# Kernel optimization log

Measured on AMD Instinct MI355X. Metric: run time of the kernel, lower is better.

Reference implementation:

```python
import jax, jax.numpy as jnp
import numpy as np


def setup_inputs() -> dict:
    key = jax.random.key(0)
    ks = jax.random.split(key, 5)
    B, N, C = 64, 384, 768
    return {
        "x": jax.random.normal(ks[0], (B, N, C), dtype=jnp.float32),
        "x_hsi": jax.random.normal(ks[1], (B, N, C), dtype=jnp.float32),
        "qkv_w": jax.random.normal(ks[2], (3 * C, C), dtype=jnp.float32) * 0.02,
        "proj_w": jax.random.normal(ks[3], (C, C), dtype=jnp.float32) * 0.02,
        "proj_b": jax.random.normal(ks[4], (C,), dtype=jnp.float32) * 0.02,
        "t_h": 8,
        "t_w": 8,
        "s_h": 16,
        "s_w": 16,
        "num_heads": 12,
    }


def reference(x, x_hsi, qkv_w, proj_w, proj_b, t_h, t_w, s_h, s_w, num_heads):
    B, N, C = x.shape
    H = num_heads
    Dh = C // H
    scale = Dh ** -0.5
    Lt = t_h * t_w * 2  # template tokens (2 templates)

    def qkv_heads(inp):
        qkv = (inp @ qkv_w.T).reshape(B, N, 3, H, Dh)
        qkv = jnp.transpose(qkv, (2, 0, 3, 1, 4))  # [3,B,H,N,Dh]
        return qkv[0], qkv[1], qkv[2]

    q, k, v = qkv_heads(x)
    q_hsi, k_hsi, v_hsi = qkv_heads(x_hsi)

    q_mt, q_s = q[:, :, :Lt], q[:, :, Lt:]
    k_mt, v_mt = k[:, :, :Lt], v[:, :, :Lt]
    q_s_hsi = q_hsi[:, :, Lt:]

    def attn(qq, kk, vv):
        a = jax.nn.softmax(jnp.einsum('bhqd,bhkd->bhqk', qq, kk) * scale, axis=-1)
        o = jnp.einsum('bhqk,bhkd->bhqd', a, vv)
        return jnp.transpose(o, (0, 2, 1, 3)).reshape(B, -1, C)

    x_mt = attn(q_mt, k_mt, v_mt)        # template-template
    x_s = attn(q_s, k, v)                # search attends to all
    x_s_hsi = attn(q_s_hsi, k_hsi, v_hsi)  # hsi search attends to all hsi

    out = jnp.concatenate([x_mt, x_s], axis=1) @ proj_w.T + proj_b
    out_hsi = jnp.concatenate([x_mt, x_s_hsi], axis=1) @ proj_w.T + proj_b
    return out, out_hsi
```

## Files before the change

kernel.cpp:

```cpp
#include <hip/hip_runtime.h>

typedef __attribute__((ext_vector_type(8))) short short8;
typedef __attribute__((ext_vector_type(4))) short bf16x4;
typedef __attribute__((ext_vector_type(4))) float f32x4;

__device__ __forceinline__ f32x4 mfma16(short8 a, short8 b, f32x4 c) {
  return __builtin_amdgcn_mfma_f32_16x16x32_bf16(a, b, c, 0, 0, 0);
}

__device__ __forceinline__ short f2bf(float f) {
  union { float f; unsigned u; } v; v.f = f;
  unsigned r = (v.u + 0x7fffu + ((v.u >> 16) & 1u)) >> 16;
  return (short)r;
}

__device__ __forceinline__ void gload16(const short* g, short* l) {
  __builtin_amdgcn_global_load_lds(
      (const __attribute__((address_space(1))) void*)g,
      (__attribute__((address_space(3))) void*)l, 16, 0, 0);
}

__global__ __launch_bounds__(256) void cvt_k(const float* __restrict__ src,
                                             short* __restrict__ dst, long n8) {
  long i = (long)blockIdx.x * 256 + threadIdx.x;
  const long stride = (long)gridDim.x * 256;
  for (; i < n8; i += stride) {
    float4 a = *(const float4*)(src + i * 8);
    float4 b = *(const float4*)(src + i * 8 + 4);
    short8 o = {f2bf(a.x), f2bf(a.y), f2bf(a.z), f2bf(a.w),
                f2bf(b.x), f2bf(b.y), f2bf(b.z), f2bf(b.w)};
    *(short8*)(dst + i * 8) = o;
  }
}

__device__ __forceinline__ void gemm256_core(
    const short* a00, const short* a01, const short* a10, const short* a11,
    const short* b00, const short* b01, const short* b10, const short* b11,
    char* lds, int wv, int lane, f32x4 (&acc)[8][4]) {
  const int l15 = lane & 15, q4 = lane >> 4;
  const int wm = wv & 1, wn = wv >> 1;
  const char* rdA = lds + wm * 16384;
  const char* rdB = lds + 32768 + (wn >> 1) * 16384;
  const int rB0 = (wn & 1) * 64;

  auto stg = [&](int T, int h, int tt) {
    const int t = tt >= 12 ? tt - 12 : tt;
    char* d = lds + (t & 1) * 65536 + T * 32768 + h * 16384 + wv * 2048;
    const short* g0 = T ? (h ? b10 : b00) : (h ? a10 : a00);
    const short* g1 = T ? (h ? b11 : b01) : (h ? a11 : a01);
    gload16(g0 + t * 64, (short*)d);
    gload16(g1 + t * 64, (short*)(d + 1024));
  };
  auto rdfrag = [&](const char* base, int rowl, int ks) -> short8 {
    int off = ks * 8192 + rowl * 64 + q4 * 16;
    off ^= ((off >> 9) & 1) << 5;
    return *(const short8*)(base + off);
  };

  stg(0, 0, 0); stg(0, 1, 0); stg(1, 0, 0); stg(1, 1, 0);
  stg(1, 0, 1); stg(1, 1, 1);
  asm volatile("s_waitcnt vmcnt(4)" ::: "memory");
  __builtin_amdgcn_s_barrier();

  auto ktile = [&](int buf, int t) {
    const char* A = rdA + buf * 65536;
    const char* B = rdB + buf * 65536;
    short8 afl[4], bfr[4][2];
#pragma unroll
    for (int m = 0; m < 4; ++m) afl[m] = rdfrag(A, m * 16 + l15, 0);
#pragma unroll
    for (int n = 0; n < 4; ++n) bfr[n][0] = rdfrag(B, rB0 + n * 16 + l15, 0);
    stg(0, 0, t + 1);
    __builtin_amdgcn_s_barrier();
    __builtin_amdgcn_s_setprio(1);
#pragma unroll
    for (int m = 0; m < 4; ++m)
#pragma unroll
      for (int n = 0; n < 4; ++n)
        acc[m][n] = mfma16(afl[m], bfr[n][0], acc[m][n]);
    __builtin_amdgcn_s_setprio(0);
    __builtin_amdgcn_s_barrier();
#pragma unroll
    for (int m = 0; m < 4; ++m) afl[m] = rdfrag(A, m * 16 + l15, 1);
#pragma unroll
    for (int n = 0; n < 4; ++n) bfr[n][1] = rdfrag(B, rB0 + n * 16 + l15, 1);
    stg(0, 1, t + 1);
    __builtin_amdgcn_s_barrier();
    __builtin_amdgcn_s_setprio(1);
#pragma unroll
    for (int m = 0; m < 4; ++m)
#pragma unroll
      for (int n = 0; n < 4; ++n)
        acc[m][n] = mfma16(afl[m], bfr[n][1], acc[m][n]);
    __builtin_amdgcn_s_setprio(0);
    __builtin_amdgcn_s_barrier();
#pragma unroll
    for (int m = 0; m < 4; ++m) afl[m] = rdfrag(A, (m + 4) * 16 + l15, 0);
    stg(1, 0, t + 2);
    __builtin_amdgcn_s_barrier();
    __builtin_amdgcn_s_setprio(1);
#pragma unroll
    for (int m = 0; m < 4; ++m)
#pragma unroll
      for (int n = 0; n < 4; ++n)
        acc[m + 4][n] = mfma16(afl[m], bfr[n][0], acc[m + 4][n]);
    __builtin_amdgcn_s_setprio(0);
    __builtin_amdgcn_s_barrier();
#pragma unroll
    for (int m = 0; m < 4; ++m) afl[m] = rdfrag(A, (m + 4) * 16 + l15, 1);
    stg(1, 1, t + 2);
    __builtin_amdgcn_s_barrier();
    __builtin_amdgcn_s_setprio(1);
#pragma unroll
    for (int m = 0; m < 4; ++m)
#pragma unroll
      for (int n = 0; n < 4; ++n)
        acc[m + 4][n] = mfma16(afl[m], bfr[n][1], acc[m + 4][n]);
    __builtin_amdgcn_s_setprio(0);
    asm volatile("s_waitcnt vmcnt(4)" ::: "memory");
    __builtin_amdgcn_s_barrier();
  };

  for (int g = 0; g < 6; ++g) {
    ktile(0, 2 * g);
    ktile(1, 2 * g + 1);
  }
}

__device__ __forceinline__ void stage_geom(int wv, int lane, int* srow, int* coff) {
#pragma unroll
  for (int j = 0; j < 2; ++j) {
    const int s = wv * 128 + j * 64 + lane;
    srow[j] = (s >> 2) & 127;
    coff[j] = (s >> 9) * 32 + (((((s & 3) << 4) ^ (((s >> 5) & 1) << 5))) >> 1);
  }
}

__global__ __launch_bounds__(512, 2) void gemm_qkv_k(
    const short* __restrict__ A0, const short* __restrict__ A1,
    const short* __restrict__ W,
    short* __restrict__ O0, short* __restrict__ O1) {
  extern __shared__ char lds[];
  const int tid = threadIdx.x, lane = tid & 63, wv = tid >> 6;
  const int l15 = lane & 15, q4 = lane >> 4;
  const int m0 = blockIdx.x * 256, n0 = blockIdx.y * 256;
  const short* A = blockIdx.z ? A1 : A0;
  short* O = blockIdx.z ? O1 : O0;

  int srow[2], coff[2];
  stage_geom(wv, lane, srow, coff);
  const short* a00 = A + (long)(m0 + srow[0]) * 768 + coff[0];
  const short* a01 = A + (long)(m0 + srow[1]) * 768 + coff[1];
  const short* a10 = A + (long)(m0 + 128 + srow[0]) * 768 + coff[0];
  const short* a11 = A + (long)(m0 + 128 + srow[1]) * 768 + coff[1];
  const short* b00 = W + (long)(n0 + srow[0]) * 768 + coff[0];
  const short* b01 = W + (long)(n0 + srow[1]) * 768 + coff[1];
  const short* b10 = W + (long)(n0 + 128 + srow[0]) * 768 + coff[0];
  const short* b11 = W + (long)(n0 + 128 + srow[1]) * 768 + coff[1];

  f32x4 acc[8][4] = {};
  gemm256_core(a00, a01, a10, a11, b00, b01, b10, b11, lds, wv, lane, acc);

  const int wm = wv & 1, wn = wv >> 1;
#pragma unroll
  for (int m = 0; m < 8; ++m)
#pragma unroll
    for (int n = 0; n < 4; ++n) {
      const int col = n0 + wn * 64 + n * 16 + l15;
#pragma unroll
      for (int r = 0; r < 4; ++r) {
        const int row = m0 + wm * 128 + m * 16 + q4 * 4 + r;
        O[(long)row * 2304 + col] = f2bf(acc[m][n][r]);
      }
    }
}

template <int NK, int QW>
__global__ __launch_bounds__(512, 2) void attn_f(
    const short* __restrict__ qkvx, const short* __restrict__ qkvh,
    short* __restrict__ omt, short* __restrict__ os, short* __restrict__ osh) {
  constexpr int KT = NK / 64;
  constexpr int MB = QW / 16;
  __shared__ __align__(16) short kk[2][64 * 72];
  __shared__ __align__(16) short vvs[2][64 * 72];
  __shared__ __align__(16) short sp[8][QW * 72];

  const int tid = threadIdx.x, lane = tid & 63, wv = tid >> 6;
  const int l15 = lane & 15, q4 = lane >> 4;
  const int b = blockIdx.x, h = blockIdx.y, kind = blockIdx.z;

  const short* src = kind ? qkvh : qkvx;
  short* outb;
  int q0;
  if (NK == 128) {
    outb = omt + ((long)b * 128) * 768 + h * 64;
    q0 = 0;
  } else {
    outb = (kind ? osh : os) + ((long)b * 256) * 768 + h * 64;
    q0 = 128;
  }
  const short* qb = src + ((long)(b * 384 + q0 + wv * QW)) * 2304 + h * 64;
  const short* kb = src + (long)b * 384 * 2304 + 768 + h * 64;
  const short* vb = kb + 768;

  const int key0 = tid >> 3, dg0 = tid & 7;

  short8 qf[MB][2];
#pragma unroll
  for (int m = 0; m < MB; ++m)
#pragma unroll
    for (int ks = 0; ks < 2; ++ks)
      qf[m][ks] = *(const short8*)(qb + (long)(m * 16 + l15) * 2304 + ks * 32 + q4 * 8);

  float mxr[MB][4], smr[MB][4];
  f32x4 oacc[MB][4] = {};
#pragma unroll
  for (int m = 0; m < MB; ++m)
#pragma unroll
    for (int r = 0; r < 4; ++r) { mxr[m][r] = -3e30f; smr[m][r] = 0.f; }

  short8 ka = *(const short8*)(kb + (long)key0 * 2304 + dg0 * 8);
  short8 va = *(const short8*)(vb + (long)key0 * 2304 + dg0 * 8);

  const float scale = 0.125f;
  char* spw = (char*)&sp[wv][0];

  for (int kt = 0; kt < KT; ++kt) {
    const int buf = kt & 1;
    *(short8*)&kk[buf][key0 * 72 + dg0 * 8] = ka;
    char* vt = (char*)&vvs[buf][0];
#pragma unroll
    for (int e = 0; e < 8; ++e) {
      const int d0 = dg0 * 8 + e;
      *(short*)(vt + ((d0 * 144 + key0 * 2) ^ (dg0 << 4))) = va[e];
    }
    __syncthreads();
    if (kt + 1 < KT) {
      ka = *(const short8*)(kb + (long)((kt + 1) * 64 + key0) * 2304 + dg0 * 8);
      va = *(const short8*)(vb + (long)((kt + 1) * 64 + key0) * 2304 + dg0 * 8);
    }

    f32x4 sacc[MB][4] = {};
#pragma unroll
    for (int n = 0; n < 4; ++n) {
      short8 kf0 = *(const short8*)&kk[buf][(n * 16 + l15) * 72 + q4 * 8];
      short8 kf1 = *(const short8*)&kk[buf][(n * 16 + l15) * 72 + 32 + q4 * 8];
#pragma unroll
      for (int m = 0; m < MB; ++m) {
        sacc[m][n] = mfma16(qf[m][0], kf0, sacc[m][n]);
        sacc[m][n] = mfma16(qf[m][1], kf1, sacc[m][n]);
      }
    }

#pragma unroll
    for (int m = 0; m < MB; ++m) {
      float pm[4];
#pragma unroll
      for (int r = 0; r < 4; ++r)
        pm[r] = fmaxf(fmaxf(sacc[m][0][r], sacc[m][1][r]),
                      fmaxf(sacc[m][2][r], sacc[m][3][r]));
#pragma unroll
      for (int r = 0; r < 4; ++r) {
        pm[r] = fmaxf(pm[r], __shfl_xor(pm[r], 1));
        pm[r] = fmaxf(pm[r], __shfl_xor(pm[r], 2));
        pm[r] = fmaxf(pm[r], __shfl_xor(pm[r], 4));
        pm[r] = fmaxf(pm[r], __shfl_xor(pm[r], 8));
      }
#pragma unroll
      for (int r = 0; r < 4; ++r) {
        const float mnew = fmaxf(mxr[m][r], pm[r]);
        const float resc = __expf((mxr[m][r] - mnew) * scale);
        mxr[m][r] = mnew;
        smr[m][r] *= resc;
#pragma unroll
        for (int n2 = 0; n2 < 4; ++n2) oacc[m][n2][r] *= resc;
      }
#pragma unroll
      for (int n = 0; n < 4; ++n)
#pragma unroll
        for (int r = 0; r < 4; ++r) {
          const float e = __expf((sacc[m][n][r] - mxr[m][r]) * scale);
          smr[m][r] += e;
          const int row = m * 16 + q4 * 4 + r;
          const int byte = (row * 144 + (n * 16 + l15) * 2) ^ (((row >> 3) & 1) << 5);
          *(short*)(spw + byte) = f2bf(e);
        }
    }

#pragma unroll
    for (int ks = 0; ks < 2; ++ks) {
      short8 pf[MB];
#pragma unroll
      for (int m = 0; m < MB; ++m) {
        const int row = m * 16 + l15;
        const int byte = (row * 144 + ks * 64 + q4 * 16) ^ (((row >> 3) & 1) << 5);
        pf[m] = *(const short8*)(spw + byte);
      }
#pragma unroll
      for (int n2 = 0; n2 < 4; ++n2) {
        const int db = n2 * 16 + l15;
        short8 vf = *(const short8*)(vt + ((db * 144 + (ks * 32 + q4 * 8) * 2) ^
                                           (((db >> 3) & 7) << 4)));
#pragma unroll
        for (int m = 0; m < MB; ++m)
          oacc[m][n2] = mfma16(pf[m], vf, oacc[m][n2]);
      }
    }
  }

  short* ob = outb + (long)wv * QW * 768;
#pragma unroll
  for (int m = 0; m < MB; ++m)
#pragma unroll
    for (int r = 0; r < 4; ++r) {
      float s = smr[m][r];
      s += __shfl_xor(s, 1);
      s += __shfl_xor(s, 2);
      s += __shfl_xor(s, 4);
      s += __shfl_xor(s, 8);
      const float inv = 1.f / s;
#pragma unroll
      for (int n2 = 0; n2 < 4; ++n2)
        ob[(m * 16 + q4 * 4 + r) * 768 + n2 * 16 + l15] = f2bf(oacc[m][n2][r] * inv);
    }
}

__global__ __launch_bounds__(512, 2) void gemm_proj_k(
    const short* __restrict__ mt, const short* __restrict__ sA,
    const short* __restrict__ sh,
    const short* __restrict__ W, const float* __restrict__ bias,
    float* __restrict__ out, int cb0) {
  extern __shared__ char lds[];
  const int tid = threadIdx.x, lane = tid & 63, wv = tid >> 6;
  const int l15 = lane & 15, q4 = lane >> 4;
  const int m0 = blockIdx.x * 256, n0 = blockIdx.y * 256;
  const short* s = blockIdx.z ? sh : sA;

  int srow[2], coff[2];
  stage_geom(wv, lane, srow, coff);
  auto arow = [&](int r) -> const short* {
    const int ba = r / 384, na = r % 384;
    return na < 128 ? (mt + ((long)ba * 128 + na) * 768)
                    : (s + ((long)ba * 256 + (na - 128)) * 768);
  };
  const short* a00 = arow(m0 + srow[0]) + coff[0];
  const short* a01 = arow(m0 + srow[1]) + coff[1];
  const short* a10 = arow(m0 + 128 + srow[0]) + coff[0];
  const short* a11 = arow(m0 + 128 + srow[1]) + coff[1];
  const short* b00 = W + (long)(n0 + srow[0]) * 768 + coff[0];
  const short* b01 = W + (long)(n0 + srow[1]) * 768 + coff[1];
  const short* b10 = W + (long)(n0 + 128 + srow[0]) * 768 + coff[0];
  const short* b11 = W + (long)(n0 + 128 + srow[1]) * 768 + coff[1];

  f32x4 acc[8][4] = {};
  gemm256_core(a00, a01, a10, a11, b00, b01, b10, b11, lds, wv, lane, acc);

  const int wm = wv & 1, wn = wv >> 1;
#pragma unroll
  for (int n = 0; n < 4; ++n) {
    const int col = n0 + wn * 64 + n * 16 + l15;
    const float bvv = bias[col];
#pragma unroll
    for (int m = 0; m < 8; ++m)
#pragma unroll
      for (int r = 0; r < 4; ++r) {
        const int row = m0 + wm * 128 + m * 16 + q4 * 4 + r;
        out[(long)blockIdx.z * 18874368 + ((long)cb0 * 384 + row) * 768 + col] =
            acc[m][n][r] + bvv;
      }
  }
}

extern "C" void kernel_launch(void* const* d_in, const int* in_sizes, int n_in,
                              void* d_out, int out_size, void* d_ws, size_t ws_size,
                              hipStream_t stream) {
  (void)in_sizes; (void)n_in; (void)out_size;
  const float* x  = (const float*)d_in[0];
  const float* xh = (const float*)d_in[1];
  const float* qw = (const float*)d_in[2];
  const float* pw = (const float*)d_in[3];
  const float* pb = (const float*)d_in[4];
  float* out = (float*)d_out;

  const long qwSz = 2304L * 768 * 2;
  const long pwSz = 768L * 768 * 2;
  const long fixedW = qwSz + pwSz;
  const long perBatch = (2L * 384 * 768 + 2L * 384 * 2304 + 640L * 768) * 2;
  int CB = 64;
  while (CB > 2 && (long)CB * perBatch + fixedW > (long)ws_size) CB >>= 1;

  char* ws = (char*)d_ws;
  short* qwbf = (short*)ws;
  short* pwbf = (short*)(ws + qwSz);
  char* dyn = ws + fixedW;
  const long xbfSz = (long)CB * 384 * 768 * 2;
  const long qkvSz = (long)CB * 384 * 2304 * 2;
  const long mtSz  = (long)CB * 128 * 768 * 2;
  const long sSz   = (long)CB * 256 * 768 * 2;
  short* xbf  = (short*)dyn;
  short* xhbf = (short*)(dyn + xbfSz);
  short* qkvx = (short*)(dyn + 2 * xbfSz);
  short* qkvh = (short*)(dyn + 2 * xbfSz + qkvSz);
  short* amt  = (short*)(dyn + 2 * xbfSz + 2 * qkvSz);
  short* as_  = (short*)(dyn + 2 * xbfSz + 2 * qkvSz + mtSz);
  short* ash  = (short*)(dyn + 2 * xbfSz + 2 * qkvSz + mtSz + sSz);

  cvt_k<<<864, 256, 0, stream>>>(qw, qwbf, 2304L * 768 / 8);
  cvt_k<<<288, 256, 0, stream>>>(pw, pwbf, 768L * 768 / 8);

  const int nch = 64 / CB;
  for (int c = 0; c < nch; ++c) {
    const int cb0 = c * CB;
    const long n8 = (long)CB * 384 * 768 / 8;
    cvt_k<<<2048, 256, 0, stream>>>(x + (long)cb0 * 384 * 768, xbf, n8);
    cvt_k<<<2048, 256, 0, stream>>>(xh + (long)cb0 * 384 * 768, xhbf, n8);
    dim3 g1((CB * 384) / 256, 9, 2);
    gemm_qkv_k<<<g1, 512, 131072, stream>>>(xbf, xhbf, qwbf, qkvx, qkvh);
    attn_f<128, 16><<<dim3(CB, 12, 1), 512, 0, stream>>>(qkvx, qkvh, amt, as_, ash);
    attn_f<384, 32><<<dim3(CB, 12, 2), 512, 0, stream>>>(qkvx, qkvh, amt, as_, ash);
    dim3 g3((CB * 384) / 256, 3, 2);
    gemm_proj_k<<<g3, 512, 131072, stream>>>(amt, as_, ash, pwbf, pb, out, cb0);
  }
}
```

Baseline: 666.3 us.

## Fuse fp32-to-bf16 activation conversion into QKV GEMM and skip softmax rescales

The QKV GEMM now reads fp32 activations directly, loading them into registers, converting them with packed bf16 conversion instructions and writing them into LDS. This removes the two separate conversion kernels and their bf16 workspace round trip. A-tile staging moves from async global-to-LDS loads to register loads plus LDS stores, which adds VGPR pressure and LDS write traffic to the GEMM. Separately, the attention softmax now rescales the running max only when some row's new max exceeds the stored max by a threshold, which avoids many exp and multiply operations but lets exponents grow without a rescale in between.

```diff
diff --git a/kernel.cpp b/kernel.cpp
--- a/kernel.cpp
+++ b/kernel.cpp
@@ -12,6 +12,12 @@
   union { float f; unsigned u; } v; v.f = f;
   unsigned r = (v.u + 0x7fffu + ((v.u >> 16) & 1u)) >> 16;
   return (short)r;
+}
+
+__device__ __forceinline__ unsigned cvtpk(float lo, float hi) {
+  unsigned r;
+  asm volatile("v_cvt_pk_bf16_f32 %0, %1, %2" : "=v"(r) : "v"(lo), "v"(hi));
+  return r;
 }
 
 __device__ __forceinline__ void gload16(const short* g, short* l) {
@@ -33,6 +39,157 @@
   }
 }
 
+__device__ __forceinline__ void stage_geom(int wv, int lane, int* srow, int* coff) {
+#pragma unroll
+  for (int j = 0; j < 2; ++j) {
+    const int s = wv * 128 + j * 64 + lane;
+    srow[j] = (s >> 2) & 127;
+    coff[j] = (s >> 9) * 32 + (((((s & 3) << 4) ^ (((s >> 5) & 1) << 5))) >> 1);
+  }
+}
+
+__global__ __launch_bounds__(512, 2) void gemm_qkv_k(
+    const float* __restrict__ A0, const float* __restrict__ A1,
+    const short* __restrict__ W,
+    short* __restrict__ O0, short* __restrict__ O1) {
+  extern __shared__ char lds[];
+  const int tid = threadIdx.x, lane = tid & 63, wv = tid >> 6;
+  const int l15 = lane & 15, q4 = lane >> 4;
+  const int m0 = blockIdx.x * 256, n0 = blockIdx.y * 256;
+  const float* A = blockIdx.z ? A1 : A0;
+  short* O = blockIdx.z ? O1 : O0;
+  const int wm = wv & 1, wn = wv >> 1;
+  const char* rdA = lds + wm * 16384;
+  const char* rdB = lds + 32768 + (wn >> 1) * 16384;
+  const int rB0 = (wn & 1) * 64;
+
+  const int arow = (tid >> 2) & 127, ac16 = tid & 3;
+  const int abase = (arow * 64 + ac16 * 16) ^ (((arow >> 3) & 1) << 5);
+  const float* asrcL = A + (long)(m0 + arow) * 768 + ac16 * 8;
+  const float* asrcH = A + (long)(m0 + 128 + arow) * 768 + ac16 * 8;
+
+  int srow[2], coff[2];
+  stage_geom(wv, lane, srow, coff);
+  const short* b00 = W + (long)(n0 + srow[0]) * 768 + coff[0];
+  const short* b01 = W + (long)(n0 + srow[1]) * 768 + coff[1];
+  const short* b10 = W + (long)(n0 + 128 + srow[0]) * 768 + coff[0];
+  const short* b11 = W + (long)(n0 + 128 + srow[1]) * 768 + coff[1];
+
+  auto stgB = [&](int h, int tt) {
+    const int t = tt >= 12 ? tt - 12 : tt;
+    char* d = lds + (t & 1) * 65536 + 32768 + h * 16384 + wv * 2048;
+    gload16((h ? b10 : b00) + t * 64, (short*)d);
+    gload16((h ? b11 : b01) + t * 64, (short*)(d + 1024));
+  };
+  float4 areg[4][2];
+  auto loadA = [&](int tt) {
+    const int t = tt >= 12 ? tt - 12 : tt;
+    const float* pL = asrcL + t * 64;
+    const float* pH = asrcH + t * 64;
+    areg[0][0] = *(const float4*)(pL);       areg[0][1] = *(const float4*)(pL + 4);
+    areg[1][0] = *(const float4*)(pL + 32);  areg[1][1] = *(const float4*)(pL + 36);
+    areg[2][0] = *(const float4*)(pH);       areg[2][1] = *(const float4*)(pH + 4);
+    areg[3][0] = *(const float4*)(pH + 32);  areg[3][1] = *(const float4*)(pH + 36);
+  };
+  auto writeA = [&](int tt) {
+    char* dstb = lds + (tt & 1) * 65536;
+#pragma unroll
+    for (int j = 0; j < 4; ++j) {
+      uint4 w;
+      w.x = cvtpk(areg[j][0].x, areg[j][0].y);
+      w.y = cvtpk(areg[j][0].z, areg[j][0].w);
+      w.z = cvtpk(areg[j][1].x, areg[j][1].y);
+      w.w = cvtpk(areg[j][1].z, areg[j][1].w);
+      *(uint4*)(dstb + ((j & 1) * 8192 + (j >> 1) * 16384 + abase)) = w;
+    }
+  };
+  auto rdfrag = [&](const char* base, int rowl, int ks) -> short8 {
+    int off = ks * 8192 + rowl * 64 + q4 * 16;
+    off ^= ((off >> 9) & 1) << 5;
+    return *(const short8*)(base + off);
+  };
+
+  stgB(0, 0); stgB(1, 0);
+  loadA(0);
+  stgB(0, 1); stgB(1, 1);
+  asm volatile("s_waitcnt vmcnt(4)" ::: "memory");
+  writeA(0);
+  asm volatile("s_waitcnt lgkmcnt(0)" ::: "memory");
+  __builtin_amdgcn_s_barrier();
+
+  f32x4 acc[8][4] = {};
+  for (int t = 0; t < 12; ++t) {
+    const int buf = t & 1;
+    const char* Ab = rdA + buf * 65536;
+    const char* Bb = rdB + buf * 65536;
+    short8 afl[4], bfr[4][2];
+#pragma unroll
+    for (int m = 0; m < 4; ++m) afl[m] = rdfrag(Ab, m * 16 + l15, 0);
+#pragma unroll
+    for (int n = 0; n < 4; ++n) bfr[n][0] = rdfrag(Bb, rB0 + n * 16 + l15, 0);
+    loadA(t + 1);
+    __builtin_amdgcn_s_barrier();
+    __builtin_amdgcn_s_setprio(1);
+#pragma unroll
+    for (int m = 0; m < 4; ++m)
+#pragma unroll
+      for (int n = 0; n < 4; ++n) acc[m][n] = mfma16(afl[m], bfr[n][0], acc[m][n]);
+    __builtin_amdgcn_s_setprio(0);
+    __builtin_amdgcn_s_barrier();
+#pragma unroll
+    for (int m = 0; m < 4; ++m) afl[m] = rdfrag(Ab, m * 16 + l15, 1);
+#pragma unroll
+    for (int n = 0; n < 4; ++n) bfr[n][1] = rdfrag(Bb, rB0 + n * 16 + l15, 1);
+    __builtin_amdgcn_s_barrier();
+    __builtin_amdgcn_s_setprio(1);
+#pragma unroll
+    for (int m = 0; m < 4; ++m)
+#pragma unroll
+      for (int n = 0; n < 4; ++n) acc[m][n] = mfma16(afl[m], bfr[n][1], acc[m][n]);
+    __builtin_amdgcn_s_setprio(0);
+    __builtin_amdgcn_s_barrier();
+#pragma unroll
+    for (int m = 0; m < 4; ++m) afl[m] = rdfrag(Ab, (m + 4) * 16 + l15, 0);
+    stgB(0, t + 2);
+    __builtin_amdgcn_s_barrier();
+    __builtin_amdgcn_s_setprio(1);
+#pragma unroll
+    for (int m = 0; m < 4; ++m)
+#pragma unroll
+      for (int n = 0; n < 4; ++n)
+        acc[m + 4][n] = mfma16(afl[m], bfr[n][0], acc[m + 4][n]);
+    __builtin_amdgcn_s_setprio(0);
+    __builtin_amdgcn_s_barrier();
+#pragma unroll
+    for (int m = 0; m < 4; ++m) afl[m] = rdfrag(Ab, (m + 4) * 16 + l15, 1);
+    stgB(1, t + 2);
+    __builtin_amdgcn_s_barrier();
+    __builtin_amdgcn_s_setprio(1);
+#pragma unroll
+    for (int m = 0; m < 4; ++m)
+#pragma unroll
+      for (int n = 0; n < 4; ++n)
+        acc[m + 4][n] = mfma16(afl[m], bfr[n][1], acc[m + 4][n]);
+    __builtin_amdgcn_s_setprio(0);
+    asm volatile("s_waitcnt vmcnt(4)" ::: "memory");
+    writeA(t + 1);
+    asm volatile("s_waitcnt lgkmcnt(0)" ::: "memory");
+    __builtin_amdgcn_s_barrier();
+  }
+
+#pragma unroll
+  for (int m = 0; m < 8; ++m)
+#pragma unroll
+    for (int n = 0; n < 4; ++n) {
+      const int col = n0 + wn * 64 + n * 16 + l15;
+#pragma unroll
+      for (int r = 0; r < 4; ++r) {
+        const int row = m0 + wm * 128 + m * 16 + q4 * 4 + r;
+        O[(long)row * 2304 + col] = f2bf(acc[m][n][r]);
+      }
+    }
+}
+
 __device__ __forceinline__ void gemm256_core(
     const short* a00, const short* a01, const short* a10, const short* a11,
     const short* b00, const short* b01, const short* b10, const short* b11,
@@ -76,8 +233,7 @@
 #pragma unroll
     for (int m = 0; m < 4; ++m)
 #pragma unroll
-      for (int n = 0; n < 4; ++n)
-        acc[m][n] = mfma16(afl[m], bfr[n][0], acc[m][n]);
+      for (int n = 0; n < 4; ++n) acc[m][n] = mfma16(afl[m], bfr[n][0], acc[m][n]);
     __builtin_amdgcn_s_setprio(0);
     __builtin_amdgcn_s_barrier();
 #pragma unroll
@@ -90,8 +246,7 @@
 #pragma unroll
     for (int m = 0; m < 4; ++m)
 #pragma unroll
-      for (int n = 0; n < 4; ++n)
-        acc[m][n] = mfma16(afl[m], bfr[n][1], acc[m][n]);
+      for (int n = 0; n < 4; ++n) acc[m][n] = mfma16(afl[m], bfr[n][1], acc[m][n]);
     __builtin_amdgcn_s_setprio(0);
     __builtin_amdgcn_s_barrier();
 #pragma unroll
@@ -125,54 +280,6 @@
     ktile(0, 2 * g);
     ktile(1, 2 * g + 1);
   }
-}
-
-__device__ __forceinline__ void stage_geom(int wv, int lane, int* srow, int* coff) {
-#pragma unroll
-  for (int j = 0; j < 2; ++j) {
-    const int s = wv * 128 + j * 64 + lane;
-    srow[j] = (s >> 2) & 127;
-    coff[j] = (s >> 9) * 32 + (((((s & 3) << 4) ^ (((s >> 5) & 1) << 5))) >> 1);
-  }
-}
-
-__global__ __launch_bounds__(512, 2) void gemm_qkv_k(
-    const short* __restrict__ A0, const short* __restrict__ A1,
-    const short* __restrict__ W,
-    short* __restrict__ O0, short* __restrict__ O1) {
-  extern __shared__ char lds[];
-  const int tid = threadIdx.x, lane = tid & 63, wv = tid >> 6;
-  const int l15 = lane & 15, q4 = lane >> 4;
-  const int m0 = blockIdx.x * 256, n0 = blockIdx.y * 256;
-  const short* A = blockIdx.z ? A1 : A0;
-  short* O = blockIdx.z ? O1 : O0;
-
-  int srow[2], coff[2];
-  stage_geom(wv, lane, srow, coff);
-  const short* a00 = A + (long)(m0 + srow[0]) * 768 + coff[0];
-  const short* a01 = A + (long)(m0 + srow[1]) * 768 + coff[1];
-  const short* a10 = A + (long)(m0 + 128 + srow[0]) * 768 + coff[0];
-  const short* a11 = A + (long)(m0 + 128 + srow[1]) * 768 + coff[1];
-  const short* b00 = W + (long)(n0 + srow[0]) * 768 + coff[0];
-  const short* b01 = W + (long)(n0 + srow[1]) * 768 + coff[1];
-  const short* b10 = W + (long)(n0 + 128 + srow[0]) * 768 + coff[0];
-  const short* b11 = W + (long)(n0 + 128 + srow[1]) * 768 + coff[1];
-
-  f32x4 acc[8][4] = {};
-  gemm256_core(a00, a01, a10, a11, b00, b01, b10, b11, lds, wv, lane, acc);
-
-  const int wm = wv & 1, wn = wv >> 1;
-#pragma unroll
-  for (int m = 0; m < 8; ++m)
-#pragma unroll
-    for (int n = 0; n < 4; ++n) {
-      const int col = n0 + wn * 64 + n * 16 + l15;
-#pragma unroll
-      for (int r = 0; r < 4; ++r) {
-        const int row = m0 + wm * 128 + m * 16 + q4 * 4 + r;
-        O[(long)row * 2304 + col] = f2bf(acc[m][n][r]);
-      }
-    }
 }
 
 template <int NK, int QW>
@@ -266,14 +373,19 @@
         pm[r] = fmaxf(pm[r], __shfl_xor(pm[r], 4));
         pm[r] = fmaxf(pm[r], __shfl_xor(pm[r], 8));
       }
-#pragma unroll
-      for (int r = 0; r < 4; ++r) {
-        const float mnew = fmaxf(mxr[m][r], pm[r]);
-        const float resc = __expf((mxr[m][r] - mnew) * scale);
-        mxr[m][r] = mnew;
-        smr[m][r] *= resc;
-#pragma unroll
-        for (int n2 = 0; n2 < 4; ++n2) oacc[m][n2][r] *= resc;
+      bool need = false;
+#pragma unroll
+      for (int r = 0; r < 4; ++r) need = need || (pm[r] > mxr[m][r] + 8.f);
+      if (__any(need)) {
+#pragma unroll
+        for (int r = 0; r < 4; ++r) {
+          const float mnew = fmaxf(mxr[m][r], pm[r]);
+          const float resc = __expf((mxr[m][r] - mnew) * scale);
+          mxr[m][r] = mnew;
+          smr[m][r] *= resc;
+#pragma unroll
+          for (int n2 = 0; n2 < 4; ++n2) oacc[m][n2][r] *= resc;
+        }
       }
 #pragma unroll
       for (int n = 0; n < 4; ++n)
@@ -385,7 +497,7 @@
   const long qwSz = 2304L * 768 * 2;
   const long pwSz = 768L * 768 * 2;
   const long fixedW = qwSz + pwSz;
-  const long perBatch = (2L * 384 * 768 + 2L * 384 * 2304 + 640L * 768) * 2;
+  const long perBatch = (2L * 384 * 2304 + 640L * 768) * 2;
   int CB = 64;
   while (CB > 2 && (long)CB * perBatch + fixedW > (long)ws_size) CB >>= 1;
 
@@ -393,17 +505,14 @@
   short* qwbf = (short*)ws;
   short* pwbf = (short*)(ws + qwSz);
   char* dyn = ws + fixedW;
-  const long xbfSz = (long)CB * 384 * 768 * 2;
   const long qkvSz = (long)CB * 384 * 2304 * 2;
   const long mtSz  = (long)CB * 128 * 768 * 2;
   const long sSz   = (long)CB * 256 * 768 * 2;
-  short* xbf  = (short*)dyn;
-  short* xhbf = (short*)(dyn + xbfSz);
-  short* qkvx = (short*)(dyn + 2 * xbfSz);
-  short* qkvh = (short*)(dyn + 2 * xbfSz + qkvSz);
-  short* amt  = (short*)(dyn + 2 * xbfSz + 2 * qkvSz);
-  short* as_  = (short*)(dyn + 2 * xbfSz + 2 * qkvSz + mtSz);
-  short* ash  = (short*)(dyn + 2 * xbfSz + 2 * qkvSz + mtSz + sSz);
+  short* qkvx = (short*)dyn;
+  short* qkvh = (short*)(dyn + qkvSz);
+  short* amt  = (short*)(dyn + 2 * qkvSz);
+  short* as_  = (short*)(dyn + 2 * qkvSz + mtSz);
+  short* ash  = (short*)(dyn + 2 * qkvSz + mtSz + sSz);
 
   cvt_k<<<864, 256, 0, stream>>>(qw, qwbf, 2304L * 768 / 8);
   cvt_k<<<288, 256, 0, stream>>>(pw, pwbf, 768L * 768 / 8);
@@ -411,11 +520,10 @@
   const int nch = 64 / CB;
   for (int c = 0; c < nch; ++c) {
     const int cb0 = c * CB;
-    const long n8 = (long)CB * 384 * 768 / 8;
-    cvt_k<<<2048, 256, 0, stream>>>(x + (long)cb0 * 384 * 768, xbf, n8);
-    cvt_k<<<2048, 256, 0, stream>>>(xh + (long)cb0 * 384 * 768, xhbf, n8);
+    const float* xA = x  + (long)cb0 * 384 * 768;
+    const float* xB = xh + (long)cb0 * 384 * 768;
     dim3 g1((CB * 384) / 256, 9, 2);
-    gemm_qkv_k<<<g1, 512, 131072, stream>>>(xbf, xhbf, qwbf, qkvx, qkvh);
+    gemm_qkv_k<<<g1, 512, 131072, stream>>>(xA, xB, qwbf, qkvx, qkvh);
     attn_f<128, 16><<<dim3(CB, 12, 1), 512, 0, stream>>>(qkvx, qkvh, amt, as_, ash);
     attn_f<384, 32><<<dim3(CB, 12, 2), 512, 0, stream>>>(qkvx, qkvh, amt, as_, ash);
     dim3 g3((CB * 384) / 256, 3, 2);
```

New measurement: 726.2 us. +9.0%, slower.
